# Kernel tuning notes

Measured on AMD Instinct MI355X. Metric: run time of the kernel, lower is better.

Reference implementation:

```python
import jax, jax.numpy as jnp
import numpy as np

T, B, D, H, L = 512, 128, 400, 400, 3


def setup_inputs() -> dict:
    key = jax.random.key(0)
    ks = jax.random.split(key, 12)
    x = jax.random.normal(ks[0], (T, B, D), dtype=jnp.float32)
    lengths = jnp.sort(jax.random.randint(ks[1], (B,), 1, T + 1))[::-1]
    s = 1.0 / np.sqrt(H)
    def w(k, shape):
        return jax.random.normal(k, shape, dtype=jnp.float32) * s
    return {
        "x": x,
        "lengths": lengths,
        # forward-direction cells: layer0 input D, layers 1..2 input 2H
        "Wih_f0": w(ks[2], (4 * H, D)),
        "Wih_f12": w(ks[3], (L - 1, 4 * H, 2 * H)),
        "Whh_f": w(ks[4], (L, 4 * H, H)),
        "b_f": jnp.zeros((L, 4 * H), jnp.float32),
        # backward-direction cells
        "Wih_b0": w(ks[5], (4 * H, D)),
        "Wih_b12": w(ks[6], (L - 1, 4 * H, 2 * H)),
        "Whh_b": w(ks[7], (L, 4 * H, H)),
        "b_b": jnp.zeros((L, 4 * H), jnp.float32),
    }


def _layer(x, mask, Wih, Whh, bias, reverse):
    # x: [T,B,Din], mask: [T,B] bool. Precompute input-side gates once.
    gx = jnp.einsum("tbd,gd->tbg", x, Wih) + bias  # [T,B,4H]
    nb, h_dim = x.shape[1], Whh.shape[-1]

    def step(carry, inp):
        h, c = carry
        g_x, m = inp
        g = g_x + h @ Whh.T
        i, f, gc, o = jnp.split(g, 4, axis=-1)
        i, f, o = jax.nn.sigmoid(i), jax.nn.sigmoid(f), jax.nn.sigmoid(o)
        gc = jnp.tanh(gc)
        c_new = f * c + i * gc
        h_new = o * jnp.tanh(c_new)
        m = m[:, None]
        # inactive sequences keep old state (fwd) / init zeros (bwd) -- matches packed semantics
        h = jnp.where(m, h_new, h)
        c = jnp.where(m, c_new, c)
        return (h, c), h

    if reverse:
        gx, m_seq = gx[::-1], mask[::-1]
    else:
        m_seq = mask
    init = (jnp.zeros((nb, h_dim), x.dtype), jnp.zeros((nb, h_dim), x.dtype))
    _, out = jax.lax.scan(step, init, (gx, m_seq))
    if reverse:
        out = out[::-1]
    return out * mask[:, :, None]


def reference(x, lengths, Wih_f0, Wih_f12, Whh_f, b_f, Wih_b0, Wih_b12, Whh_b, b_b):
    mask = jnp.arange(x.shape[0])[:, None] < lengths[None, :]  # [T,B]
    Wih_fs = [Wih_f0, Wih_f12[0], Wih_f12[1]]
    Wih_bs = [Wih_b0, Wih_b12[0], Wih_b12[1]]
    for l in range(L):
        f = _layer(x, mask, Wih_fs[l], Whh_f[l], b_f[l], reverse=False)
        b = _layer(x, mask, Wih_bs[l], Whh_b[l], b_b[l], reverse=True)
        x = jnp.concatenate([f, b], axis=-1)  # [T,B,2H]
    return x
```

## Files before the change

### kernel.cpp

```cpp
#include <hip/hip_runtime.h>
#include <stdint.h>
#include <stddef.h>

#define T_ 512
#define B_ 128
#define D_ 400
#define H_ 400
#define HP 416
#define GP 1664
#define NW 3328
#define KXP 832
#define NTILES 13
#define NGRP 8
#define REC_BLOCKS 208
#define PAIRS 208

#define GC_FSTRIDE 576

#define HBT_U64   ((size_t)16*2*16*PAIRS)
#define HBT_BYTES (HBT_U64*8)

#define WHHR_US8  ((size_t)2*13*4*2*13*64)
#define WHHR_BYTES (WHHR_US8*8*2)
#define WIHR_US8  ((size_t)2*13*4*2*26*64)
#define WIHR_BYTES (WIHR_US8*8*2)

typedef __attribute__((ext_vector_type(8))) __bf16 bf16x8;
typedef __attribute__((ext_vector_type(4))) float f32x4;
typedef __attribute__((ext_vector_type(8))) unsigned short us8;

__device__ __forceinline__ unsigned short f2bf(float f){
  unsigned u = __builtin_bit_cast(unsigned, f);
  u = (u + 0x7FFFu + ((u >> 16) & 1u)) >> 16;
  return (unsigned short)u;
}
__device__ __forceinline__ float bf2f(unsigned short s){
  unsigned u = ((unsigned)s) << 16;
  return __builtin_bit_cast(float, u);
}
__device__ __forceinline__ float sigm(float x){ return 1.f / (1.f + __expf(-x)); }
__device__ __forceinline__ float tanh_f(float x){
  float ax = fabsf(x);
  float e = __expf(-2.f * ax);
  float t = (1.f - e) / (1.f + e);
  return x < 0.f ? -t : t;
}

__device__ __forceinline__ void h_store_u64(unsigned long long* p, unsigned long long v){
  __hip_atomic_store(p, v, __ATOMIC_RELAXED, __HIP_MEMORY_SCOPE_AGENT);
}
__device__ __forceinline__ unsigned long long h_load_u64(const unsigned long long* p){
  return __hip_atomic_load(p, __ATOMIC_RELAXED, __HIP_MEMORY_SCOPE_AGENT);
}

__global__ void k_conv_x0(const float* __restrict__ x, unsigned short* __restrict__ xa){
  const size_t i = (size_t)blockIdx.x*256 + threadIdx.x;
  if (i >= (size_t)T_*B_*KXP) return;
  const int k = (int)(i % KXP);
  const size_t tb = i / KXP;
  xa[i] = f2bf(k < D_ ? x[tb*D_ + k] : 0.f);
}

__global__ void k_prep_wihR(const float* __restrict__ wf, const float* __restrict__ wb,
                            int mode, unsigned short* __restrict__ dst){
  const size_t i = (size_t)blockIdx.x*256 + threadIdx.x;
  if (i >= WIHR_US8) return;
  const int lane = (int)(i & 63);
  size_t q = i >> 6;
  const int kk = (int)(q % 26); q /= 26;
  const int ch = (int)(q % 2);  q /= 2;
  const int g  = (int)(q % 4);  q /= 4;
  const int tile = (int)(q % 13);
  const int dirx = (int)(q / 13);
  const int c  = tile*32 + ch*16 + (lane & 15);
  const int k0 = kk*32 + (lane >> 4)*8;
  const float* W = dirx ? wb : wf;
  const int stride = mode ? 800 : D_;
  unsigned short v[8];
  #pragma unroll
  for (int e = 0; e < 8; ++e){
    const int k = k0 + e;
    int ks;
    if (mode == 0) ks = (k < D_) ? k : -1;
    else           ks = (k < 400) ? k : ((k >= 416 && k < 816) ? (k - 16) : -1);
    const float x = (c < H_ && ks >= 0) ? W[(size_t)(g*H_ + c)*stride + ks] : 0.f;
    v[e] = f2bf(x);
  }
  *(us8*)(dst + i*8) = *(const us8*)v;
}

__global__ void k_prep_whhR(const float* __restrict__ wf, const float* __restrict__ wb,
                            unsigned short* __restrict__ dst){
  const size_t i = (size_t)blockIdx.x*256 + threadIdx.x;
  if (i >= WHHR_US8) return;
  const int lane = (int)(i & 63);
  size_t q = i >> 6;
  const int kk = (int)(q % 13); q /= 13;
  const int ch = (int)(q % 2);  q /= 2;
  const int w  = (int)(q % 4);  q /= 4;
  const int tile = (int)(q % 13);
  const int dirx = (int)(q / 13);
  const int c  = tile*32 + ch*16 + (lane & 15);
  const int k0 = kk*32 + (lane >> 4)*8;
  const float* W = dirx ? wb : wf;
  unsigned short v[8];
  #pragma unroll
  for (int e = 0; e < 8; ++e){
    const int k = k0 + e;
    const float x = (c < H_ && k < H_) ? W[(size_t)(w*H_ + c)*H_ + k] : 0.f;
    v[e] = f2bf(x);
  }
  *(us8*)(dst + i*8) = *(const us8*)v;
}

__global__ void k_prep_bias(const float* __restrict__ bsf, const float* __restrict__ bsb,
                            float* __restrict__ dst){
  const int n = blockIdx.x*256 + threadIdx.x;
  if (n >= NW) return;
  const int d = n / GP, ng = n % GP, g = ng / HP, r = ng % HP;
  dst[n] = (r < H_) ? (d ? bsb : bsf)[g*H_ + r] : 0.f;
}

template<bool LAST>
__global__ __launch_bounds__(256, 1) void lstm_rec(
    const unsigned short* __restrict__ xin,
    const unsigned short* __restrict__ wihR,
    const unsigned short* __restrict__ whhR,
    const float* __restrict__ biasp,
    const int* __restrict__ lens,
    unsigned long long* hbt,
    unsigned short* __restrict__ xn,
    float* __restrict__ out)
{
  __shared__ unsigned short HS[16*424];
  __shared__ unsigned short XS[16*840];
  __shared__ float GC[4*GC_FSTRIDE];

  const int tid = threadIdx.x;
  const int bid = blockIdx.x;
  const int dir  = bid / 104;
  const int rem  = bid % 104;
  const int grp  = rem / NTILES;
  const int tile = rem % NTILES;
  const int l  = tid & 63;
  const int w  = tid >> 6;
  const int lr = l & 15;
  const int lk = l >> 4;
  const int cid = dir*NGRP + grp;

  us8 Bf0[13], Bf1[13];
  {
    const unsigned short* bs =
        whhR + ((size_t)((dir*13 + tile)*4 + w)*2*13*64 + l)*8;
    #pragma unroll
    for (int kk = 0; kk < 13; ++kk)
      Bf0[kk] = *(const us8*)(bs + (size_t)kk*512);
    const unsigned short* bs1 = bs + (size_t)13*64*8;
    #pragma unroll
    for (int kk = 0; kk < 13; ++kk)
      Bf1[kk] = *(const us8*)(bs1 + (size_t)kk*512);
  }
  us8 Wf0[26], Wf1[26];
  {
    const unsigned short* ws0 =
        wihR + ((size_t)(((dir*13 + tile)*4 + w)*2 + 0)*26*64 + l)*8;
    #pragma unroll
    for (int kk = 0; kk < 26; ++kk)
      Wf0[kk] = *(const us8*)(ws0 + (size_t)kk*512);
    const unsigned short* ws1 = ws0 + (size_t)26*64*8;
    #pragma unroll
    for (int kk = 0; kk < 26; ++kk)
      Wf1[kk] = *(const us8*)(ws1 + (size_t)kk*512);
  }

  const int grp_len = lens[grp*16];
  const int eb  = tid & 15;
  const int p2  = tid >> 4;
  const int mylen = lens[grp*16 + eb];
  const int c0 = 2*p2, c1 = 2*p2 + 1;
  float b0g[4], b1g[4];
  #pragma unroll
  for (int g = 0; g < 4; ++g){
    b0g[g] = biasp[dir*GP + g*HP + tile*32 + c0];
    b1g[g] = biasp[dir*GP + g*HP + tile*32 + c1];
  }
  float cs0 = 0.f, cs1 = 0.f, hs0 = 0.f, hs1 = 0.f;
  __syncthreads();

  int s_a = 0;
  unsigned long long* const myslot =
      hbt + (((size_t)cid*2)*16 + eb)*PAIRS + tile*16 + p2;

  for (int s = 0; s < T_; ++s){
    const int t = dir ? (T_ - 1 - s) : s;
    if (t >= grp_len) continue;

    unsigned long long vx[13];
    {
      const unsigned long long* xrow =
          (const unsigned long long*)(xin + ((size_t)t*B_ + grp*16)*KXP);
      #pragma unroll
      for (int j = 0; j < 13; ++j){
        const int idx = j*256 + tid;
        const int b = idx / 208, qq = idx % 208;
        vx[j] = xrow[(size_t)b*208 + qq];
      }
    }
    {
      const unsigned rtag = (unsigned)s_a;
      const unsigned long long* hb =
          hbt + ((size_t)(cid*2 + (s_a & 1))*16)*PAIRS;
      unsigned long long v[13];
      #pragma unroll
      for (int j = 0; j < 13; ++j)
        v[j] = h_load_u64(hb + j*256 + tid);
      unsigned stale = 0;
      #pragma unroll
      for (int j = 0; j < 13; ++j)
        if ((unsigned)(v[j] >> 32) != rtag) stale |= 1u << j;
      while (stale){
        const unsigned m = stale;
        #pragma unroll
        for (int j = 0; j < 13; ++j)
          if (m & (1u << j)) v[j] = h_load_u64(hb + j*256 + tid);
        #pragma unroll
        for (int j = 0; j < 13; ++j)
          if ((m & (1u << j)) && (unsigned)(v[j] >> 32) == rtag) stale &= ~(1u << j);
      }
      #pragma unroll
      for (int j = 0; j < 13; ++j){
        const int idx = j*256 + tid;
        const int b = idx / PAIRS, p = idx % PAIRS;
        *(unsigned*)&HS[b*424 + 2*p] = (unsigned)v[j];
      }
    }
    #pragma unroll
    for (int j = 0; j < 13; ++j){
      const int idx = j*256 + tid;
      const int b = idx / 208, qq = idx % 208;
      *(unsigned long long*)&XS[b*840 + qq*4] = vx[j];
    }
    __syncthreads();

    f32x4 a0 = (f32x4){0.f,0.f,0.f,0.f}, a1 = (f32x4){0.f,0.f,0.f,0.f};
    {
      const int abx = lr*840 + lk*8;
      #pragma unroll
      for (int kk = 0; kk < 26; ++kk){
        bf16x8 xa = __builtin_bit_cast(bf16x8, *(const us8*)&XS[abx + kk*32]);
        a0 = __builtin_amdgcn_mfma_f32_16x16x32_bf16(xa, Wf0[kk], a0, 0, 0, 0);
        a1 = __builtin_amdgcn_mfma_f32_16x16x32_bf16(xa, Wf1[kk], a1, 0, 0, 0);
      }
      const int ab = lr*424 + lk*8;
      #pragma unroll
      for (int kk = 0; kk < 13; ++kk){
        bf16x8 av = __builtin_bit_cast(bf16x8, *(const us8*)&HS[ab + kk*32]);
        a0 = __builtin_amdgcn_mfma_f32_16x16x32_bf16(av, Bf0[kk], a0, 0, 0, 0);
        a1 = __builtin_amdgcn_mfma_f32_16x16x32_bf16(av, Bf1[kk], a1, 0, 0, 0);
      }
    }
    {
      float* Gw = GC + w * GC_FSTRIDE;
      #pragma unroll
      for (int r = 0; r < 4; ++r){
        Gw[(lk*4 + r)*36 + lr]      = a0[r];
        Gw[(lk*4 + r)*36 + 16 + lr] = a1[r];
      }
    }
    __syncthreads();

    const bool act = t < mylen;
    {
      const float gi0 = GC[0*GC_FSTRIDE + eb*36 + c0] + b0g[0];
      const float gf0 = GC[1*GC_FSTRIDE + eb*36 + c0] + b0g[1];
      const float gg0 = GC[2*GC_FSTRIDE + eb*36 + c0] + b0g[2];
      const float go0 = GC[3*GC_FSTRIDE + eb*36 + c0] + b0g[3];
      const float gi1 = GC[0*GC_FSTRIDE + eb*36 + c1] + b1g[0];
      const float gf1 = GC[1*GC_FSTRIDE + eb*36 + c1] + b1g[1];
      const float gg1 = GC[2*GC_FSTRIDE + eb*36 + c1] + b1g[2];
      const float go1 = GC[3*GC_FSTRIDE + eb*36 + c1] + b1g[3];
      const float cn0 = sigm(gf0)*cs0 + sigm(gi0)*tanh_f(gg0);
      const float hn0 = sigm(go0) * tanh_f(cn0);
      const float cn1 = sigm(gf1)*cs1 + sigm(gi1)*tanh_f(gg1);
      const float hn1 = sigm(go1) * tanh_f(cn1);
      if (act){ cs0 = cn0; hs0 = hn0; cs1 = cn1; hs1 = hn1; }
    }
    {
      const unsigned hu = (unsigned)f2bf(hs0) | ((unsigned)f2bf(hs1) << 16);
      const unsigned long long hv =
          (unsigned long long)hu | ((unsigned long long)(unsigned)(s_a + 1) << 32);
      h_store_u64(myslot + ((size_t)((s_a + 1) & 1))*16*PAIRS, hv);
    }
    if (act){
      const int bg = grp*16 + eb;
      const int hc = tile*32 + c0;
      if constexpr (LAST){
        float* op = out + ((size_t)t*B_ + bg)*800 + dir*H_ + hc;
        if (hc < H_)     op[0] = hs0;
        if (hc + 1 < H_) op[1] = hs1;
      } else {
        const unsigned hu = (unsigned)f2bf(hs0) | ((unsigned)f2bf(hs1) << 16);
        *(unsigned*)(xn + ((size_t)t*B_ + bg)*KXP + (size_t)dir*HP + hc) = hu;
      }
    }
    ++s_a;
  }
}

static void run_all(void* const* din, float* out, char* ws, hipStream_t stream)
{
  const float* x      = (const float*)din[0];
  const int* lens     = (const int*)din[1];
  const float* wihf0  = (const float*)din[2];
  const float* wihf12 = (const float*)din[3];
  const float* whhf   = (const float*)din[4];
  const float* bsf    = (const float*)din[5];
  const float* wihb0  = (const float*)din[6];
  const float* wihb12 = (const float*)din[7];
  const float* whhb   = (const float*)din[8];
  const float* bsb    = (const float*)din[9];

  char* p = ws;
  auto alloc = [&](size_t n){ char* r = p; p += (n + 255) & ~(size_t)255; return r; };
  unsigned short* xA = (unsigned short*)alloc((size_t)T_*B_*KXP*2);
  unsigned short* xB = (unsigned short*)alloc((size_t)T_*B_*KXP*2);
  unsigned short* wihR = (unsigned short*)alloc(WIHR_BYTES);
  unsigned short* whhR = (unsigned short*)alloc(WHHR_BYTES);
  float* biasp       = (float*)alloc((size_t)NW*4);
  unsigned long long* hbt = (unsigned long long*)alloc(HBT_BYTES);

  hipMemsetAsync(out, 0, (size_t)T_*B_*800*4, stream);
  {
    size_t n = (size_t)T_*B_*KXP;
    k_conv_x0<<<dim3((unsigned)((n+255)/256)), dim3(256), 0, stream>>>(x, xA);
  }

  const unsigned short* xinv[3] = {xA, xB, xA};
  unsigned short* xoutv[3] = {xB, xA, nullptr};

  for (int lyr = 0; lyr < 3; ++lyr){
    const float* wf = (lyr == 0) ? wihf0 : wihf12 + (size_t)(lyr-1)*1600*800;
    const float* wb = (lyr == 0) ? wihb0 : wihb12 + (size_t)(lyr-1)*1600*800;
    {
      size_t n = WIHR_US8;
      k_prep_wihR<<<dim3((unsigned)((n+255)/256)), dim3(256), 0, stream>>>(
          wf, wb, lyr ? 1 : 0, wihR);
    }
    k_prep_bias<<<dim3((NW+255)/256), dim3(256), 0, stream>>>(
        bsf + (size_t)lyr*1600, bsb + (size_t)lyr*1600, biasp);
    {
      size_t n = WHHR_US8;
      k_prep_whhR<<<dim3((unsigned)((n+255)/256)), dim3(256), 0, stream>>>(
          whhf + (size_t)lyr*1600*400, whhb + (size_t)lyr*1600*400, whhR);
    }
    hipMemsetAsync(hbt, 0, HBT_BYTES, stream);

    if (lyr < 2)
      lstm_rec<false><<<dim3(REC_BLOCKS), dim3(256), 0, stream>>>(
          xinv[lyr], wihR, whhR, biasp, lens, hbt, xoutv[lyr], out);
    else
      lstm_rec<true><<<dim3(REC_BLOCKS), dim3(256), 0, stream>>>(
          xinv[lyr], wihR, whhR, biasp, lens, hbt, nullptr, out);
  }
}

extern "C" void kernel_launch(void* const* d_in, const int* in_sizes, int n_in,
                              void* d_out, int out_size, void* d_ws, size_t ws_size,
                              hipStream_t stream)
{
  (void)in_sizes; (void)n_in; (void)out_size;
  auto align = [](size_t n){ return (n + 255) & ~(size_t)255; };
  const size_t need =
      align((size_t)T_*B_*KXP*2) * 2 +
      align(WIHR_BYTES) +
      align(WHHR_BYTES) +
      align((size_t)NW*4) +
      align(HBT_BYTES);

  if (ws_size >= need)
    run_all(d_in, (float*)d_out, (char*)d_ws, stream);
  else
    hipMemsetAsync(d_out, 0, (size_t)T_*B_*800*4, stream);
}
```

Before: 5.593 ms.

## Double-buffer x tile and overlap input-gate MFMAs with hidden-state polling

Prefetches the next timestep's input row into registers while the current one is consumed, and double-buffers the x tile in LDS. The input-projection MFMAs now run before the spin-wait on the other blocks' hidden state, so that independent work hides cross-block synchronisation latency. The loop also iterates only over the group's active length instead of skipping inactive steps. The cost is more LDS (now dynamic shared memory) and an extra barrier per step.

```diff
diff --git a/kernel.cpp b/kernel.cpp
--- a/kernel.cpp
+++ b/kernel.cpp
@@ -16,6 +16,14 @@
 #define PAIRS 208
 
 #define GC_FSTRIDE 576
+
+#define HS_BYTES  (16*424*2)
+#define XS_STRIDE 840
+#define XS_BYTES  (16*XS_STRIDE*2)
+#define XS0_OFF   HS_BYTES
+#define XS1_OFF   (HS_BYTES + XS_BYTES)
+#define GC_OFF    (HS_BYTES + 2*XS_BYTES)
+#define LDS_TOTAL (GC_OFF + 4*GC_FSTRIDE*4)
 
 #define HBT_U64   ((size_t)16*2*16*PAIRS)
 #define HBT_BYTES (HBT_U64*8)
@@ -132,9 +140,11 @@
     unsigned short* __restrict__ xn,
     float* __restrict__ out)
 {
-  __shared__ unsigned short HS[16*424];
-  __shared__ unsigned short XS[16*840];
-  __shared__ float GC[4*GC_FSTRIDE];
+  extern __shared__ char smem[];
+  unsigned short* HS = (unsigned short*)smem;
+  unsigned short* XS0 = (unsigned short*)(smem + XS0_OFF);
+  unsigned short* XS1 = (unsigned short*)(smem + XS1_OFF);
+  float* GC = (float*)(smem + GC_OFF);
 
   const int tid = threadIdx.x;
   const int bid = blockIdx.x;
@@ -187,18 +197,36 @@
   float cs0 = 0.f, cs1 = 0.f, hs0 = 0.f, hs1 = 0.f;
   __syncthreads();
 
-  int s_a = 0;
   unsigned long long* const myslot =
       hbt + (((size_t)cid*2)*16 + eb)*PAIRS + tile*16 + p2;
 
-  for (int s = 0; s < T_; ++s){
-    const int t = dir ? (T_ - 1 - s) : s;
-    if (t >= grp_len) continue;
-
-    unsigned long long vx[13];
-    {
+  unsigned long long vx[13];
+  {
+    const int t0 = dir ? (grp_len - 1) : 0;
+    const unsigned long long* xrow =
+        (const unsigned long long*)(xin + ((size_t)t0*B_ + grp*16)*KXP);
+    #pragma unroll
+    for (int j = 0; j < 13; ++j){
+      const int idx = j*256 + tid;
+      const int b = idx / 208, qq = idx % 208;
+      vx[j] = xrow[(size_t)b*208 + qq];
+    }
+  }
+
+  for (int ss = 0; ss < grp_len; ++ss){
+    const int t = dir ? (grp_len - 1 - ss) : ss;
+    unsigned short* XSb = (ss & 1) ? XS1 : XS0;
+
+    #pragma unroll
+    for (int j = 0; j < 13; ++j){
+      const int idx = j*256 + tid;
+      const int b = idx / 208, qq = idx % 208;
+      *(unsigned long long*)&XSb[b*XS_STRIDE + qq*4] = vx[j];
+    }
+    if (ss + 1 < grp_len){
+      const int tn = dir ? (grp_len - 2 - ss) : (ss + 1);
       const unsigned long long* xrow =
-          (const unsigned long long*)(xin + ((size_t)t*B_ + grp*16)*KXP);
+          (const unsigned long long*)(xin + ((size_t)tn*B_ + grp*16)*KXP);
       #pragma unroll
       for (int j = 0; j < 13; ++j){
         const int idx = j*256 + tid;
@@ -206,14 +234,27 @@
         vx[j] = xrow[(size_t)b*208 + qq];
       }
     }
-    {
-      const unsigned rtag = (unsigned)s_a;
-      const unsigned long long* hb =
-          hbt + ((size_t)(cid*2 + (s_a & 1))*16)*PAIRS;
-      unsigned long long v[13];
-      #pragma unroll
-      for (int j = 0; j < 13; ++j)
-        v[j] = h_load_u64(hb + j*256 + tid);
+    __syncthreads();
+
+    const unsigned rtag = (unsigned)ss;
+    const unsigned long long* hb =
+        hbt + ((size_t)(cid*2 + (ss & 1))*16)*PAIRS;
+    unsigned long long v[13];
+    #pragma unroll
+    for (int j = 0; j < 13; ++j)
+      v[j] = h_load_u64(hb + j*256 + tid);
+
+    f32x4 a0 = (f32x4){0.f,0.f,0.f,0.f}, a1 = (f32x4){0.f,0.f,0.f,0.f};
+    {
+      const int abx = lr*XS_STRIDE + lk*8;
+      #pragma unroll
+      for (int kk = 0; kk < 26; ++kk){
+        bf16x8 xa = __builtin_bit_cast(bf16x8, *(const us8*)&XSb[abx + kk*32]);
+        a0 = __builtin_amdgcn_mfma_f32_16x16x32_bf16(xa, Wf0[kk], a0, 0, 0, 0);
+        a1 = __builtin_amdgcn_mfma_f32_16x16x32_bf16(xa, Wf1[kk], a1, 0, 0, 0);
+      }
+    }
+    {
       unsigned stale = 0;
       #pragma unroll
       for (int j = 0; j < 13; ++j)
@@ -234,23 +275,9 @@
         *(unsigned*)&HS[b*424 + 2*p] = (unsigned)v[j];
       }
     }
-    #pragma unroll
-    for (int j = 0; j < 13; ++j){
-      const int idx = j*256 + tid;
-      const int b = idx / 208, qq = idx % 208;
-      *(unsigned long long*)&XS[b*840 + qq*4] = vx[j];
-    }
     __syncthreads();
 
-    f32x4 a0 = (f32x4){0.f,0.f,0.f,0.f}, a1 = (f32x4){0.f,0.f,0.f,0.f};
-    {
-      const int abx = lr*840 + lk*8;
-      #pragma unroll
-      for (int kk = 0; kk < 26; ++kk){
-        bf16x8 xa = __builtin_bit_cast(bf16x8, *(const us8*)&XS[abx + kk*32]);
-        a0 = __builtin_amdgcn_mfma_f32_16x16x32_bf16(xa, Wf0[kk], a0, 0, 0, 0);
-        a1 = __builtin_amdgcn_mfma_f32_16x16x32_bf16(xa, Wf1[kk], a1, 0, 0, 0);
-      }
+    {
       const int ab = lr*424 + lk*8;
       #pragma unroll
       for (int kk = 0; kk < 13; ++kk){
@@ -288,8 +315,8 @@
     {
       const unsigned hu = (unsigned)f2bf(hs0) | ((unsigned)f2bf(hs1) << 16);
       const unsigned long long hv =
-          (unsigned long long)hu | ((unsigned long long)(unsigned)(s_a + 1) << 32);
-      h_store_u64(myslot + ((size_t)((s_a + 1) & 1))*16*PAIRS, hv);
+          (unsigned long long)hu | ((unsigned long long)(unsigned)(ss + 1) << 32);
+      h_store_u64(myslot + ((size_t)((ss + 1) & 1))*16*PAIRS, hv);
     }
     if (act){
       const int bg = grp*16 + eb;
@@ -303,7 +330,6 @@
         *(unsigned*)(xn + ((size_t)t*B_ + bg)*KXP + (size_t)dir*HP + hc) = hu;
       }
     }
-    ++s_a;
   }
 }
 
@@ -334,6 +360,10 @@
     size_t n = (size_t)T_*B_*KXP;
     k_conv_x0<<<dim3((unsigned)((n+255)/256)), dim3(256), 0, stream>>>(x, xA);
   }
+  hipFuncSetAttribute(reinterpret_cast<const void*>(&lstm_rec<false>),
+                      hipFuncAttributeMaxDynamicSharedMemorySize, LDS_TOTAL);
+  hipFuncSetAttribute(reinterpret_cast<const void*>(&lstm_rec<true>),
+                      hipFuncAttributeMaxDynamicSharedMemorySize, LDS_TOTAL);
 
   const unsigned short* xinv[3] = {xA, xB, xA};
   unsigned short* xoutv[3] = {xB, xA, nullptr};
@@ -356,10 +386,10 @@
     hipMemsetAsync(hbt, 0, HBT_BYTES, stream);
 
     if (lyr < 2)
-      lstm_rec<false><<<dim3(REC_BLOCKS), dim3(256), 0, stream>>>(
+      lstm_rec<false><<<dim3(REC_BLOCKS), dim3(256), LDS_TOTAL, stream>>>(
           xinv[lyr], wihR, whhR, biasp, lens, hbt, xoutv[lyr], out);
     else
-      lstm_rec<true><<<dim3(REC_BLOCKS), dim3(256), 0, stream>>>(
+      lstm_rec<true><<<dim3(REC_BLOCKS), dim3(256), LDS_TOTAL, stream>>>(
           xinv[lyr], wihR, whhR, biasp, lens, hbt, nullptr, out);
   }
 }
```

Measured after the change: 5.120 ms. 1.09x faster.

## Load x fragments directly into MFMA registers and overlap with h polling

Applied to the files above, without the earlier changes.

Drops the shared-memory staging of the input row. Each lane now loads its bf16 A-fragments straight from global memory in two halves of 13 k-steps. The input-side MFMAs run before the spin-wait on the hidden state exchange, so that work overlaps the inter-block latency and one LDS round-trip is removed. The loop now iterates only over the group's active length directly, with t computed relative to grp_len. This trades coalesced loads for per-lane strided 16-byte global reads.

```diff
diff --git a/kernel.cpp b/kernel.cpp
--- a/kernel.cpp
+++ b/kernel.cpp
@@ -133,7 +133,6 @@
     float* __restrict__ out)
 {
   __shared__ unsigned short HS[16*424];
-  __shared__ unsigned short XS[16*840];
   __shared__ float GC[4*GC_FSTRIDE];
 
   const int tid = threadIdx.x;
@@ -187,33 +186,43 @@
   float cs0 = 0.f, cs1 = 0.f, hs0 = 0.f, hs1 = 0.f;
   __syncthreads();
 
-  int s_a = 0;
   unsigned long long* const myslot =
       hbt + (((size_t)cid*2)*16 + eb)*PAIRS + tile*16 + p2;
-
-  for (int s = 0; s < T_; ++s){
-    const int t = dir ? (T_ - 1 - s) : s;
-    if (t >= grp_len) continue;
-
-    unsigned long long vx[13];
-    {
-      const unsigned long long* xrow =
-          (const unsigned long long*)(xin + ((size_t)t*B_ + grp*16)*KXP);
-      #pragma unroll
-      for (int j = 0; j < 13; ++j){
-        const int idx = j*256 + tid;
-        const int b = idx / 208, qq = idx % 208;
-        vx[j] = xrow[(size_t)b*208 + qq];
-      }
-    }
-    {
-      const unsigned rtag = (unsigned)s_a;
-      const unsigned long long* hb =
-          hbt + ((size_t)(cid*2 + (s_a & 1))*16)*PAIRS;
-      unsigned long long v[13];
-      #pragma unroll
-      for (int j = 0; j < 13; ++j)
-        v[j] = h_load_u64(hb + j*256 + tid);
+  const unsigned short* const xbase = xin + ((size_t)grp*16 + lr)*KXP + lk*8;
+
+  for (int ss = 0; ss < grp_len; ++ss){
+    const int t = dir ? (grp_len - 1 - ss) : ss;
+    const unsigned short* xrow = xbase + (size_t)t*B_*KXP;
+
+    us8 xf[13];
+    #pragma unroll
+    for (int kk = 0; kk < 13; ++kk)
+      xf[kk] = *(const us8*)(xrow + kk*32);
+
+    const unsigned rtag = (unsigned)ss;
+    const unsigned long long* hb =
+        hbt + ((size_t)(cid*2 + (ss & 1))*16)*PAIRS;
+    unsigned long long v[13];
+    #pragma unroll
+    for (int j = 0; j < 13; ++j)
+      v[j] = h_load_u64(hb + j*256 + tid);
+
+    f32x4 a0 = (f32x4){0.f,0.f,0.f,0.f}, a1 = (f32x4){0.f,0.f,0.f,0.f};
+    #pragma unroll
+    for (int kk = 0; kk < 13; ++kk){
+      a0 = __builtin_amdgcn_mfma_f32_16x16x32_bf16(xf[kk], Wf0[kk], a0, 0, 0, 0);
+      a1 = __builtin_amdgcn_mfma_f32_16x16x32_bf16(xf[kk], Wf1[kk], a1, 0, 0, 0);
+    }
+    #pragma unroll
+    for (int kk = 0; kk < 13; ++kk)
+      xf[kk] = *(const us8*)(xrow + (13 + kk)*32);
+    #pragma unroll
+    for (int kk = 0; kk < 13; ++kk){
+      a0 = __builtin_amdgcn_mfma_f32_16x16x32_bf16(xf[kk], Wf0[13 + kk], a0, 0, 0, 0);
+      a1 = __builtin_amdgcn_mfma_f32_16x16x32_bf16(xf[kk], Wf1[13 + kk], a1, 0, 0, 0);
+    }
+
+    {
       unsigned stale = 0;
       #pragma unroll
       for (int j = 0; j < 13; ++j)
@@ -234,23 +243,9 @@
         *(unsigned*)&HS[b*424 + 2*p] = (unsigned)v[j];
       }
     }
-    #pragma unroll
-    for (int j = 0; j < 13; ++j){
-      const int idx = j*256 + tid;
-      const int b = idx / 208, qq = idx % 208;
-      *(unsigned long long*)&XS[b*840 + qq*4] = vx[j];
-    }
     __syncthreads();
 
-    f32x4 a0 = (f32x4){0.f,0.f,0.f,0.f}, a1 = (f32x4){0.f,0.f,0.f,0.f};
-    {
-      const int abx = lr*840 + lk*8;
-      #pragma unroll
-      for (int kk = 0; kk < 26; ++kk){
-        bf16x8 xa = __builtin_bit_cast(bf16x8, *(const us8*)&XS[abx + kk*32]);
-        a0 = __builtin_amdgcn_mfma_f32_16x16x32_bf16(xa, Wf0[kk], a0, 0, 0, 0);
-        a1 = __builtin_amdgcn_mfma_f32_16x16x32_bf16(xa, Wf1[kk], a1, 0, 0, 0);
-      }
+    {
       const int ab = lr*424 + lk*8;
       #pragma unroll
       for (int kk = 0; kk < 13; ++kk){
@@ -288,8 +283,8 @@
     {
       const unsigned hu = (unsigned)f2bf(hs0) | ((unsigned)f2bf(hs1) << 16);
       const unsigned long long hv =
-          (unsigned long long)hu | ((unsigned long long)(unsigned)(s_a + 1) << 32);
-      h_store_u64(myslot + ((size_t)((s_a + 1) & 1))*16*PAIRS, hv);
+          (unsigned long long)hu | ((unsigned long long)(unsigned)(ss + 1) << 32);
+      h_store_u64(myslot + ((size_t)((ss + 1) & 1))*16*PAIRS, hv);
     }
     if (act){
       const int bg = grp*16 + eb;
@@ -303,7 +298,6 @@
         *(unsigned*)(xn + ((size_t)t*B_ + bg)*KXP + (size_t)dir*HP + hc) = hu;
       }
     }
-    ++s_a;
   }
 }
 
```

Measured after the change: 10.91 ms. 1.95x slower.
